# Optimization experiments

Hardware: AMD Instinct MI355X
Metric: run time of the kernel (lower is better)

The kernel has to match this reference:

```python
import jax, jax.numpy as jnp
import numpy as np

N = 8_000_000
THETA_W = 1.9  # physics-loss weight in forward()
EPS_DPDT = 1e-12
# Fixed config: bulk_modulus_model='tangent' (non-const), air_dissolution_model='on', air_fraction>0


def _drho_mix_dp(p, rho_L_atm, beta_L_atm, beta_gain, air_fraction, rho_g_atm,
                 polytropic_index, p_atm, p_crit, p_min):
    # mixture_density_derivative, vectorized over p (shape [N,1])
    p_used = jnp.maximum(p, p_min)
    L = p_crit - p_atm
    x = (p_used - p_atm) / L
    theta_mid = 1.0 - 3.0 * x**2 + 2.0 * x**3           # smoothstep between p_atm and p_crit
    theta = jnp.where(p_used <= p_atm, 1.0,
                      jnp.where(p_used >= p_crit, 0.0, theta_mid))
    dtheta_mid = 6.0 * (p_used - p_atm) * (p_used - p_crit) / L**3
    dtheta_dp = jnp.where((p_used <= p_atm) | (p_used >= p_crit), 0.0, dtheta_mid)

    afr = air_fraction / (1.0 - air_fraction)
    pr = (p_atm / p_used) ** (1.0 / polytropic_index)
    p_denom = afr * pr * theta
    p_ratio = afr * pr * (theta / (p_used * polytropic_index) - dtheta_dp)

    base = 1.0 + beta_gain * (p_used - p_atm) / beta_L_atm
    exp_term = base ** (-1.0 - 1.0 / beta_gain) / beta_L_atm

    rho_mix_init = rho_L_atm + rho_g_atm * afr
    denom = beta_L_atm * exp_term * base + p_denom
    return rho_mix_init * (exp_term + p_ratio) / denom**2


def setup_inputs() -> dict:
    key = jax.random.key(0)
    k1, k2, k3, k4 = jax.random.split(key, 4)
    outputs_P = jax.random.uniform(k1, (N, 1), dtype=jnp.float32) * 50.0  # p = 0.1*outputs_P in [0,5) MPa
    targets_P = outputs_P + 0.1 * jax.random.normal(k2, (N, 1), dtype=jnp.float32)
    dpdt = 0.5 * jax.random.normal(k3, (N, 1), dtype=jnp.float32)
    mdot_A = 0.01 * jax.random.normal(k4, (N, 1), dtype=jnp.float32)
    return {
        "targets_P": targets_P,
        "dpdt": dpdt,
        "mdot_A": mdot_A,
        "V": jnp.float32(1e-3),
        "outputs_P": outputs_P,
        "rho_L_atm": jnp.float32(850.0),
        "beta_L_atm": jnp.float32(1500.0),   # MPa
        "beta_gain": jnp.float32(10.0),
        "air_fraction": jnp.float32(0.005),
        "rho_g_atm": jnp.float32(1.2),
        "polytropic_index": jnp.float32(1.4),
        "p_atm": jnp.float32(0.101325),       # MPa
        "p_crit": jnp.float32(3.0),           # MPa
        "p_min": jnp.float32(0.01),           # MPa
    }


def reference(targets_P, dpdt, mdot_A, V, outputs_P, rho_L_atm, beta_L_atm,
              beta_gain, air_fraction, rho_g_atm, polytropic_index, p_atm,
              p_crit, p_min):
    drho = _drho_mix_dp(outputs_P * 0.1, rho_L_atm, beta_L_atm, beta_gain,
                        air_fraction, rho_g_atm, polytropic_index,
                        p_atm, p_crit, p_min)                      # [N,1]
    loss_physics = jnp.abs(V * drho * dpdt - mdot_A)                # [N,1]
    loss_M = jnp.abs(outputs_P - targets_P)                         # [N,1]
    per_sample = loss_M + THETA_W * loss_physics
    mask = jnp.abs(dpdt) >= EPS_DPDT                                # skip ~zero dpdt samples
    return jnp.sum(jnp.where(mask, per_sample, 0.0))
```

## Files before the change

### kernel.cpp

```cpp
#include <hip/hip_runtime.h>

#define THREADS 256
#define NWAVES  (THREADS / 64)
#define CHUNKS  2

struct Consts {
    float p_min, p_atm, p_crit;
    float invL;
    float c_dth;
    float afr;
    float inv_n;
    float bg_over_bL;
    float inv_bL;
    float rho_mix_init;
    float V;
    float log2_patm;
    float pc1, pc2, pc3, pc4;
};

__device__ __forceinline__ float pow1p(float u, const Consts& c) {
    return fmaf(u, fmaf(u, fmaf(u, fmaf(u, c.pc4, c.pc3), c.pc2), c.pc1), 1.0f);
}

__device__ __forceinline__ float loss_elem(float oP, float tP, float dp, float md,
                                           const Consts& c) {
    float p  = 0.1f * oP;
    float pu = fmaxf(p, c.p_min);
    float dpa = pu - c.p_atm;
    float x = dpa * c.invL;
    float theta_mid = fmaf(x * x, fmaf(2.0f, x, -3.0f), 1.0f);
    bool lo = (pu <= c.p_atm);
    bool hi = (pu >= c.p_crit);
    float theta  = lo ? 1.0f : (hi ? 0.0f : theta_mid);
    float dtheta = (lo || hi) ? 0.0f : c.c_dth * dpa * (pu - c.p_crit);

    float inv_pu = __builtin_amdgcn_rcpf(pu);
    float lg_pu = __builtin_amdgcn_logf(pu);
    float pr = __builtin_amdgcn_exp2f(c.inv_n * (c.log2_patm - lg_pu));
    float apr = c.afr * pr;
    float p_denom = apr * theta;
    float p_ratio = apr * fmaf(theta * c.inv_n, inv_pu, -dtheta);

    float u  = dpa * c.bg_over_bL;
    float pb = pow1p(u, c);
    float exp_term = pb * c.inv_bL;
    float denom = fmaf(pb, u, pb) + p_denom;
    float inv_denom = __builtin_amdgcn_rcpf(denom);
    float drho = c.rho_mix_init * (exp_term + p_ratio) * inv_denom * inv_denom;

    float lp = fabsf(fmaf(c.V * dp, drho, -md));
    float lm = fabsf(oP - tP);
    float res = fmaf(1.9f, lp, lm);
    return (fabsf(dp) >= 1e-12f) ? res : 0.0f;
}

__device__ __forceinline__ float quad(const float4& o, const float4& t,
                                      const float4& d, const float4& m,
                                      const Consts& c) {
    return loss_elem(o.x, t.x, d.x, m.x, c)
         + loss_elem(o.y, t.y, d.y, m.y, c)
         + loss_elem(o.z, t.z, d.z, m.z, c)
         + loss_elem(o.w, t.w, d.w, m.w, c);
}

__device__ __forceinline__ Consts make_consts(
    const float* sV, const float* s_rhoL, const float* s_betaL,
    const float* s_bgain, const float* s_airfr, const float* s_rhog,
    const float* s_poly, const float* s_patm, const float* s_pcrit,
    const float* s_pmin) {
    Consts c;
    float beta_L = *s_betaL;
    float bgain  = *s_bgain;
    float airfr  = *s_airfr;
    float poly   = *s_poly;
    float patm   = *s_patm;
    float pcrit  = *s_pcrit;
    float L = pcrit - patm;
    c.p_min = *s_pmin;
    c.p_atm = patm;
    c.p_crit = pcrit;
    c.invL = 1.0f / L;
    c.c_dth = 6.0f / (L * L * L);
    c.afr = airfr / (1.0f - airfr);
    c.inv_n = 1.0f / poly;
    c.bg_over_bL = bgain / beta_L;
    c.inv_bL = 1.0f / beta_L;
    c.rho_mix_init = fmaf(*s_rhog, c.afr, *s_rhoL);
    c.V = *sV;
    c.log2_patm = __builtin_amdgcn_logf(patm);
    float a = -1.0f - 1.0f / bgain;
    c.pc1 = a;
    c.pc2 = a * (a - 1.0f) * 0.5f;
    c.pc3 = c.pc2 * (a - 2.0f) * (1.0f / 3.0f);
    c.pc4 = c.pc3 * (a - 3.0f) * 0.25f;
    return c;
}

__global__ __launch_bounds__(THREADS, 4) void loss_kernel(
    const float* __restrict__ targets_P,
    const float* __restrict__ dpdt,
    const float* __restrict__ mdot_A,
    const float* __restrict__ outputs_P,
    const float* __restrict__ sV,
    const float* __restrict__ s_rhoL,
    const float* __restrict__ s_betaL,
    const float* __restrict__ s_bgain,
    const float* __restrict__ s_airfr,
    const float* __restrict__ s_rhog,
    const float* __restrict__ s_poly,
    const float* __restrict__ s_patm,
    const float* __restrict__ s_pcrit,
    const float* __restrict__ s_pmin,
    float* __restrict__ partials,
    int n, int nfull)
{
    const int n4 = n >> 2;
    const float4* o4 = (const float4*)outputs_P;
    const float4* t4 = (const float4*)targets_P;
    const float4* d4 = (const float4*)dpdt;
    const float4* m4 = (const float4*)mdot_A;

    float acc = 0.0f;

    if ((int)blockIdx.x < nfull) {
        const int s0 = blockIdx.x * (THREADS * CHUNKS) + threadIdx.x;
        const int s1 = s0 + THREADS;
        float4 oa = o4[s0], ta = t4[s0], da = d4[s0], ma = m4[s0];
        float4 ob = o4[s1], tb = t4[s1], db = d4[s1], mb = m4[s1];

        const Consts c = make_consts(sV, s_rhoL, s_betaL, s_bgain, s_airfr,
                                     s_rhog, s_poly, s_patm, s_pcrit, s_pmin);
        acc += quad(oa, ta, da, ma, c);
        acc += quad(ob, tb, db, mb, c);
    } else {
        const Consts c = make_consts(sV, s_rhoL, s_betaL, s_bgain, s_airfr,
                                     s_rhog, s_poly, s_patm, s_pcrit, s_pmin);
        for (int idx = nfull * (THREADS * CHUNKS) + threadIdx.x; idx < n4;
             idx += THREADS) {
            float4 oo = o4[idx], tt = t4[idx], dd = d4[idx], mm = m4[idx];
            acc += quad(oo, tt, dd, mm, c);
        }
        for (int j = (n4 << 2) + threadIdx.x; j < n; j += THREADS) {
            acc += loss_elem(outputs_P[j], targets_P[j], dpdt[j], mdot_A[j], c);
        }
    }

    for (int off = 32; off > 0; off >>= 1)
        acc += __shfl_down(acc, off, 64);
    int lane = threadIdx.x & 63, wid = threadIdx.x >> 6;
    if (lane == 0)
        partials[blockIdx.x * NWAVES + wid] = acc;
}

__global__ __launch_bounds__(256) void loss_final_kernel(
    const float* __restrict__ partials, float* __restrict__ out, int nparts)
{
    double acc = 0.0;
    for (int i = threadIdx.x; i < nparts; i += blockDim.x)
        acc += (double)partials[i];
    for (int off = 32; off > 0; off >>= 1)
        acc += __shfl_down(acc, off, 64);
    __shared__ double wsum[4];
    int lane = threadIdx.x & 63, wid = threadIdx.x >> 6;
    if (lane == 0) wsum[wid] = acc;
    __syncthreads();
    if (threadIdx.x == 0) {
        double s = 0.0;
        #pragma unroll
        for (int w = 0; w < 4; ++w) s += wsum[w];
        out[0] = (float)s;
    }
}

extern "C" void kernel_launch(void* const* d_in, const int* in_sizes, int n_in,
                              void* d_out, int out_size, void* d_ws, size_t ws_size,
                              hipStream_t stream) {
    const float* targets_P = (const float*)d_in[0];
    const float* dpdt      = (const float*)d_in[1];
    const float* mdot_A    = (const float*)d_in[2];
    const float* sV        = (const float*)d_in[3];
    const float* outputs_P = (const float*)d_in[4];
    const float* s_rhoL    = (const float*)d_in[5];
    const float* s_betaL   = (const float*)d_in[6];
    const float* s_bgain   = (const float*)d_in[7];
    const float* s_airfr   = (const float*)d_in[8];
    const float* s_rhog    = (const float*)d_in[9];
    const float* s_poly    = (const float*)d_in[10];
    const float* s_patm    = (const float*)d_in[11];
    const float* s_pcrit   = (const float*)d_in[12];
    const float* s_pmin    = (const float*)d_in[13];

    int n  = in_sizes[0];
    int n4 = n >> 2;
    int nfull = n4 / (THREADS * CHUNKS);
    int nblocks = nfull + 1;
    int nparts = nblocks * NWAVES;

    float* partials = (float*)d_ws;

    loss_kernel<<<nblocks, THREADS, 0, stream>>>(
        targets_P, dpdt, mdot_A, outputs_P,
        sV, s_rhoL, s_betaL, s_bgain, s_airfr, s_rhog, s_poly,
        s_patm, s_pcrit, s_pmin,
        partials, n, nfull);

    loss_final_kernel<<<1, 256, 0, stream>>>(partials, (float*)d_out, nparts);
}
```

Before: 181.6 us.

## Double-buffer input tiles into LDS via global_load_lds in single-wave blocks

Replaces the one-shot 256-thread blocks with 64-thread single-wave blocks that each process a contiguous range of 256-element tiles. Loads go straight into LDS with global_load_lds, double-buffered, so the fetch of the next tile overlaps compute on the current one. The grid is capped at a fixed block count and the partial-sum layout moves to one value per block. The aim is to hide memory latency with software pipelining, at the cost of lower per-block occupancy and a reliance on the compiler placing the right waits before each LDS read.

```diff
diff --git a/kernel.cpp b/kernel.cpp
--- a/kernel.cpp
+++ b/kernel.cpp
@@ -1,20 +1,16 @@
 #include <hip/hip_runtime.h>
 
-#define THREADS 256
-#define NWAVES  (THREADS / 64)
-#define CHUNKS  2
+#define WTHREADS 64
+#define TILE_ELEMS 256
+#define NB_TARGET 6250
+
+typedef __attribute__((address_space(1))) const void ga_void;
+typedef __attribute__((address_space(3))) void ls_void;
 
 struct Consts {
     float p_min, p_atm, p_crit;
-    float invL;
-    float c_dth;
-    float afr;
-    float inv_n;
-    float bg_over_bL;
-    float inv_bL;
-    float rho_mix_init;
-    float V;
-    float log2_patm;
+    float invL, c_dth, afr, inv_n, bg_over_bL, inv_bL;
+    float rho_mix_init, V, log2_patm;
     float pc1, pc2, pc3, pc4;
 };
 
@@ -69,16 +65,10 @@
     const float* s_poly, const float* s_patm, const float* s_pcrit,
     const float* s_pmin) {
     Consts c;
-    float beta_L = *s_betaL;
-    float bgain  = *s_bgain;
-    float airfr  = *s_airfr;
-    float poly   = *s_poly;
-    float patm   = *s_patm;
-    float pcrit  = *s_pcrit;
+    float beta_L = *s_betaL, bgain = *s_bgain, airfr = *s_airfr;
+    float poly = *s_poly, patm = *s_patm, pcrit = *s_pcrit;
     float L = pcrit - patm;
-    c.p_min = *s_pmin;
-    c.p_atm = patm;
-    c.p_crit = pcrit;
+    c.p_min = *s_pmin; c.p_atm = patm; c.p_crit = pcrit;
     c.invL = 1.0f / L;
     c.c_dth = 6.0f / (L * L * L);
     c.afr = airfr / (1.0f - airfr);
@@ -96,7 +86,7 @@
     return c;
 }
 
-__global__ __launch_bounds__(THREADS, 4) void loss_kernel(
+__global__ __launch_bounds__(WTHREADS) void loss_kernel(
     const float* __restrict__ targets_P,
     const float* __restrict__ dpdt,
     const float* __restrict__ mdot_A,
@@ -112,44 +102,80 @@
     const float* __restrict__ s_pcrit,
     const float* __restrict__ s_pmin,
     float* __restrict__ partials,
-    int n, int nfull)
+    int n, int NB, int ntiles)
 {
+    __shared__ float4 bufA[4][WTHREADS];
+    __shared__ float4 bufB[4][WTHREADS];
+
+    const int lane = threadIdx.x;
     const int n4 = n >> 2;
-    const float4* o4 = (const float4*)outputs_P;
-    const float4* t4 = (const float4*)targets_P;
-    const float4* d4 = (const float4*)dpdt;
-    const float4* m4 = (const float4*)mdot_A;
+
+    const Consts c = make_consts(sV, s_rhoL, s_betaL, s_bgain, s_airfr,
+                                 s_rhog, s_poly, s_patm, s_pcrit, s_pmin);
 
     float acc = 0.0f;
 
-    if ((int)blockIdx.x < nfull) {
-        const int s0 = blockIdx.x * (THREADS * CHUNKS) + threadIdx.x;
-        const int s1 = s0 + THREADS;
-        float4 oa = o4[s0], ta = t4[s0], da = d4[s0], ma = m4[s0];
-        float4 ob = o4[s1], tb = t4[s1], db = d4[s1], mb = m4[s1];
-
-        const Consts c = make_consts(sV, s_rhoL, s_betaL, s_bgain, s_airfr,
-                                     s_rhog, s_poly, s_patm, s_pcrit, s_pmin);
-        acc += quad(oa, ta, da, ma, c);
-        acc += quad(ob, tb, db, mb, c);
+    if ((int)blockIdx.x < NB) {
+        const int base = ntiles / NB, rem = ntiles % NB;
+        const int b = blockIdx.x;
+        const int cnt   = base + (b < rem ? 1 : 0);
+        const int start = b * base + (b < rem ? b : rem);
+
+        #define STAGE(tile, BUF)                                               \
+            do {                                                               \
+                size_t _off = (size_t)(tile) * TILE_ELEMS + (size_t)lane * 4;  \
+                __builtin_amdgcn_global_load_lds((ga_void*)(outputs_P + _off), \
+                    (ls_void*)&BUF[0][0], 16, 0, 0);                           \
+                __builtin_amdgcn_global_load_lds((ga_void*)(targets_P + _off), \
+                    (ls_void*)&BUF[1][0], 16, 0, 0);                           \
+                __builtin_amdgcn_global_load_lds((ga_void*)(dpdt + _off),      \
+                    (ls_void*)&BUF[2][0], 16, 0, 0);                           \
+                __builtin_amdgcn_global_load_lds((ga_void*)(mdot_A + _off),    \
+                    (ls_void*)&BUF[3][0], 16, 0, 0);                           \
+            } while (0)
+
+        #define CONSUME(BUF)                                                   \
+            do {                                                               \
+                float4 _o = BUF[0][lane];                                      \
+                float4 _t = BUF[1][lane];                                      \
+                float4 _d = BUF[2][lane];                                      \
+                float4 _m = BUF[3][lane];                                      \
+                acc += quad(_o, _t, _d, _m, c);                                \
+            } while (0)
+
+        if (cnt > 0) {
+            STAGE(start, bufA);
+            int i = 0;
+            while (true) {
+                if (i + 1 < cnt) STAGE(start + i + 1, bufB);
+                CONSUME(bufA);
+                if (++i >= cnt) break;
+                if (i + 1 < cnt) STAGE(start + i + 1, bufA);
+                CONSUME(bufB);
+                if (++i >= cnt) break;
+            }
+        }
+        #undef STAGE
+        #undef CONSUME
     } else {
-        const Consts c = make_consts(sV, s_rhoL, s_betaL, s_bgain, s_airfr,
-                                     s_rhog, s_poly, s_patm, s_pcrit, s_pmin);
-        for (int idx = nfull * (THREADS * CHUNKS) + threadIdx.x; idx < n4;
-             idx += THREADS) {
+        const float4* o4 = (const float4*)outputs_P;
+        const float4* t4 = (const float4*)targets_P;
+        const float4* d4 = (const float4*)dpdt;
+        const float4* m4 = (const float4*)mdot_A;
+        for (int idx = ntiles * (TILE_ELEMS / 4) + lane; idx < n4;
+             idx += WTHREADS) {
             float4 oo = o4[idx], tt = t4[idx], dd = d4[idx], mm = m4[idx];
             acc += quad(oo, tt, dd, mm, c);
         }
-        for (int j = (n4 << 2) + threadIdx.x; j < n; j += THREADS) {
+        for (int j = (n4 << 2) + lane; j < n; j += WTHREADS) {
             acc += loss_elem(outputs_P[j], targets_P[j], dpdt[j], mdot_A[j], c);
         }
     }
 
     for (int off = 32; off > 0; off >>= 1)
         acc += __shfl_down(acc, off, 64);
-    int lane = threadIdx.x & 63, wid = threadIdx.x >> 6;
     if (lane == 0)
-        partials[blockIdx.x * NWAVES + wid] = acc;
+        partials[blockIdx.x] = acc;
 }
 
 __global__ __launch_bounds__(256) void loss_final_kernel(
@@ -192,17 +218,18 @@
 
     int n  = in_sizes[0];
     int n4 = n >> 2;
-    int nfull = n4 / (THREADS * CHUNKS);
-    int nblocks = nfull + 1;
-    int nparts = nblocks * NWAVES;
+    int ntiles = n4 / (TILE_ELEMS / 4);
+    int NB = ntiles < NB_TARGET ? (ntiles > 0 ? ntiles : 0) : NB_TARGET;
+    if (NB < 1) NB = 1;
+    int nblocks = NB + 1;
 
     float* partials = (float*)d_ws;
 
-    loss_kernel<<<nblocks, THREADS, 0, stream>>>(
+    loss_kernel<<<nblocks, WTHREADS, 0, stream>>>(
         targets_P, dpdt, mdot_A, outputs_P,
         sV, s_rhoL, s_betaL, s_bgain, s_airfr, s_rhog, s_poly,
         s_patm, s_pcrit, s_pmin,
-        partials, n, nfull);
-
-    loss_final_kernel<<<1, 256, 0, stream>>>(partials, (float*)d_out, nparts);
-}
+        partials, n, NB, ntiles);
+
+    loss_final_kernel<<<1, 256, 0, stream>>>(partials, (float*)d_out, nblocks);
+}
```

New measurement: 175.7 us. -3.2%, faster.
